# Performance work log

Measured on AMD Instinct MI355X. Metric: run time of the kernel, lower is better.

The kernel has to match this reference:

```python
import jax, jax.numpy as jnp
import numpy as np

K = 20          # neighbors
EPS = 1e-5      # BatchNorm eps (eval mode, running_mean=0, running_var=1)
SLOPE = 0.01    # LeakyReLU default negative_slope


def lrelu(v):
    return jnp.where(v >= 0, v, SLOPE * v)


def bn4d(y, g, b):  # y: (B, C, N, k) or (B, C, N)
    shape = (1, g.shape[0]) + (1,) * (y.ndim - 2)
    return y * (g / jnp.sqrt(1.0 + EPS)).reshape(shape) + b.reshape(shape)


def knn_idx(x, k):  # x: (B, C, N) -> (B, N, k) indices of k nearest points
    xx = jnp.sum(x * x, axis=1)                      # (B, N)
    inner = jnp.einsum('bcn,bcm->bnm', x, x)         # (B, N, N)
    dist = 2.0 * inner - xx[:, :, None] - xx[:, None, :]  # = -||xi-xj||^2
    _, idx = jax.lax.top_k(dist, k)
    return idx


def graph_feature(x, k):  # x: (B, C, N) -> (B, 2C, N, k)
    idx = knn_idx(x, k)                              # (B, N, k)
    xt = jnp.transpose(x, (0, 2, 1))                 # (B, N, C)
    nbr = jax.vmap(lambda p, i: p[i])(xt, idx)       # (B, N, k, C) gather
    ctr = xt[:, :, None, :]                          # (B, N, 1, C)
    feat = jnp.concatenate([nbr - ctr, jnp.broadcast_to(ctr, nbr.shape)], axis=-1)
    return jnp.transpose(feat, (0, 3, 1, 2))         # (B, 2C, N, k)


def edge_conv(x, w, g, b, bias=None):  # 1x1 conv + BN(eval) + LeakyReLU + max over k
    f = graph_feature(x, K)                          # (B, 2C, N, k)
    y = jnp.einsum('oc,bcnk->bonk', w, f)
    if bias is not None:
        y = y + bias.reshape(1, -1, 1, 1)
    return jnp.max(lrelu(bn4d(y, g, b)), axis=-1)    # (B, O, N)


def setup_inputs() -> dict:
    key = jax.random.key(0)
    ks = jax.random.split(key, 24)
    W = lambda k_, o, c: jax.random.normal(k_, (o, c), jnp.float32) / np.sqrt(c)
    g = lambda k_, c: 1.0 + 0.1 * jax.random.normal(k_, (c,), jnp.float32)
    bt = lambda k_, c: 0.1 * jax.random.normal(k_, (c,), jnp.float32)
    return {
        'x': jax.random.normal(ks[0], (8, 1024, 3), jnp.float32),
        'conv1_w': W(ks[1], 64, 6), 'conv1_b': bt(ks[2], 64),
        'bn1_g': g(ks[3], 64), 'bn1_b': bt(ks[4], 64),
        'conv2_w': W(ks[5], 64, 128), 'bn2_g': g(ks[6], 64), 'bn2_b': bt(ks[7], 64),
        'conv3_w': W(ks[8], 128, 128), 'bn3_g': g(ks[9], 128), 'bn3_b': bt(ks[10], 128),
        'conv4_w': W(ks[11], 256, 256), 'bn4_g': g(ks[12], 256), 'bn4_b': bt(ks[13], 256),
        'conv5_w': W(ks[14], 1024, 512),
        'lin1_w': W(ks[15], 512, 1024), 'bn6_g': g(ks[16], 512), 'bn6_b': bt(ks[17], 512),
        'lin2_w': W(ks[18], 256, 512), 'lin2_b': bt(ks[19], 256),
        'bn7_g': g(ks[20], 256), 'bn7_b': bt(ks[21], 256),
        'lin3_w': W(ks[22], 40, 256), 'lin3_b': bt(ks[23], 40),
    }


def reference(x, conv1_w, conv1_b, bn1_g, bn1_b, conv2_w, bn2_g, bn2_b,
              conv3_w, bn3_g, bn3_b, conv4_w, bn4_g, bn4_b, conv5_w,
              lin1_w, bn6_g, bn6_b, lin2_w, lin2_b, bn7_g, bn7_b, lin3_w, lin3_b):
    p = jnp.transpose(x, (0, 2, 1))                  # (B, 3, N)
    x1 = edge_conv(p, conv1_w, bn1_g, bn1_b, bias=conv1_b)   # (B, 64, N)
    x2 = edge_conv(x1, conv2_w, bn2_g, bn2_b)                # (B, 64, N)
    x3 = edge_conv(x2, conv3_w, bn3_g, bn3_b)                # (B, 128, N)
    x4 = edge_conv(x3, conv4_w, bn4_g, bn4_b)                # (B, 256, N)
    xc = jnp.concatenate([x1, x2, x3, x4], axis=1)           # (B, 512, N)
    e = jnp.einsum('oc,bcn->bon', conv5_w, xc)               # (B, 1024, N); bn5 unused in original forward
    gpool = jnp.max(e, axis=-1)                              # (B, 1024) adaptive_max_pool1d(1)
    y = gpool @ lin1_w.T
    y = lrelu(y * (bn6_g / jnp.sqrt(1.0 + EPS)) + bn6_b)     # dropout = identity (eval)
    y = y @ lin2_w.T + lin2_b
    y = lrelu(y * (bn7_g / jnp.sqrt(1.0 + EPS)) + bn7_b)
    return y @ lin3_w.T + lin3_b                             # (B, num_classes)
```

## Files before the change

### kernel.cpp

```cpp
#include <hip/hip_runtime.h>
#include <cmath>
#include <cstdint>
#include <cstddef>

#define NB 8
#define NPTS 1024
#define BN (NB*NPTS)
#define KNN 20
#define XC_C 512
#define BN_SC 0.99999500003749973f

static __device__ __forceinline__ float lrelu(float z) { return z >= 0.f ? z : 0.01f * z; }

template<int CTRL>
static __device__ __forceinline__ void dpp_max2(unsigned& loA, unsigned& hiA,
                                                unsigned& loB, unsigned& hiB) {
    unsigned tlA = (unsigned)__builtin_amdgcn_update_dpp(0, (int)loA, CTRL, 0xF, 0xF, false);
    unsigned thA = (unsigned)__builtin_amdgcn_update_dpp(0, (int)hiA, CTRL, 0xF, 0xF, false);
    unsigned tlB = (unsigned)__builtin_amdgcn_update_dpp(0, (int)loB, CTRL, 0xF, 0xF, false);
    unsigned thB = (unsigned)__builtin_amdgcn_update_dpp(0, (int)hiB, CTRL, 0xF, 0xF, false);
    unsigned long long a = ((unsigned long long)hiA << 32) | loA;
    unsigned long long b = ((unsigned long long)thA << 32) | tlA;
    if (b > a) { loA = tlA; hiA = thA; }
    unsigned long long c = ((unsigned long long)hiB << 32) | loB;
    unsigned long long d = ((unsigned long long)thB << 32) | tlB;
    if (d > c) { loB = tlB; hiB = thB; }
}

static __device__ __forceinline__ void wave_max_u64_x2(unsigned long long vA, unsigned long long vB,
                                                       unsigned long long& winA, unsigned long long& winB) {
    unsigned loA = (unsigned)vA, hiA = (unsigned)(vA >> 32);
    unsigned loB = (unsigned)vB, hiB = (unsigned)(vB >> 32);
    dpp_max2<0x121>(loA, hiA, loB, hiB);
    dpp_max2<0x122>(loA, hiA, loB, hiB);
    dpp_max2<0x124>(loA, hiA, loB, hiB);
    dpp_max2<0x128>(loA, hiA, loB, hiB);
    dpp_max2<0x142>(loA, hiA, loB, hiB);
    dpp_max2<0x143>(loA, hiA, loB, hiB);
    unsigned wloA = (unsigned)__builtin_amdgcn_readlane((int)loA, 63);
    unsigned whiA = (unsigned)__builtin_amdgcn_readlane((int)hiA, 63);
    unsigned wloB = (unsigned)__builtin_amdgcn_readlane((int)loB, 63);
    unsigned whiB = (unsigned)__builtin_amdgcn_readlane((int)hiB, 63);
    winA = ((unsigned long long)whiA << 32) | wloA;
    winB = ((unsigned long long)whiB << 32) | wloB;
}

static __device__ __forceinline__ unsigned long long shflx64(unsigned long long v, int m) {
    int lo = __shfl_xor((int)(unsigned)v, m);
    int hi = __shfl_xor((int)(unsigned)(v >> 32), m);
    return ((unsigned long long)(unsigned)hi << 32) | (unsigned)lo;
}

static __device__ __forceinline__ unsigned long long rdlane64(unsigned long long v, int l) {
    unsigned lo = (unsigned)__builtin_amdgcn_readlane((int)(unsigned)v, l);
    unsigned hi = (unsigned)__builtin_amdgcn_readlane((int)(unsigned)(v >> 32), l);
    return ((unsigned long long)hi << 32) | lo;
}

static __device__ __forceinline__ void bitonic64_desc_x2(unsigned long long& vA,
                                                         unsigned long long& vB, int lane) {
#pragma unroll
    for (int k = 2; k <= 64; k <<= 1) {
#pragma unroll
        for (int j = k >> 1; j > 0; j >>= 1) {
            unsigned long long pA = shflx64(vA, j);
            unsigned long long pB = shflx64(vB, j);
            bool takeMax = (((lane & k) == 0) == ((lane & j) == 0));
            vA = ((pA > vA) == takeMax) ? pA : vA;
            vB = ((pB > vB) == takeMax) ? pB : vB;
        }
    }
}

static __device__ __forceinline__ unsigned short f2bf(float f) {
    unsigned u = __float_as_uint(f);
    unsigned r = u + 0x7fffu + ((u >> 16) & 1u);
    return (unsigned short)(r >> 16);
}
static __device__ __forceinline__ float bf2f(unsigned short h) {
    return __uint_as_float(((unsigned)h) << 16);
}

typedef __attribute__((ext_vector_type(8))) short short8;
typedef __attribute__((ext_vector_type(4))) float floatx4;

__global__ void prep_k(const float* __restrict__ x, float* __restrict__ ft, float* __restrict__ nrm) {
    int i = blockIdx.x * 256 + threadIdx.x;
    if (i >= BN) return;
    int b = i >> 10, n = i & 1023;
    float a = x[3*i], c = x[3*i+1], d = x[3*i+2];
    float* fb = ft + (size_t)b * 3 * NPTS;
    fb[n] = a; fb[NPTS + n] = c; fb[2*NPTS + n] = d;
    nrm[i] = a*a + c*c + d*d;
}

template<int C>
__global__ __launch_bounds__(256) void knn_k(const float* __restrict__ ft,
                                             const float* __restrict__ frow, int frs,
                                             const float* __restrict__ nrm,
                                             int* __restrict__ idx) {
    __shared__ unsigned long long cand[4][2][64];
    int w = threadIdx.x >> 6;
    int lane = threadIdx.x & 63;
    int rA = blockIdx.x * 8 + 2 * w;
    int rB = rA + 1;
    int b = rA >> 10;
    const float* ftb = ft + (size_t)b * C * NPTS;

    float4 accA[4], accB[4];
#pragma unroll
    for (int j = 0; j < 4; j++) { accA[j] = make_float4(0.f,0.f,0.f,0.f); accB[j] = make_float4(0.f,0.f,0.f,0.f); }

    if constexpr ((C & 3) == 0) {
        const float4* crA = (const float4*)(frow + (size_t)rA * frs);
        const float4* crB = (const float4*)(frow + (size_t)rB * frs);
        for (int c4 = 0; c4 < C/4; c4++) {
            float4 ctA = crA[c4], ctB = crB[c4];
#pragma unroll
            for (int cc = 0; cc < 4; cc++) {
                float cA = (&ctA.x)[cc], cB = (&ctB.x)[cc];
                const float4* rm = (const float4*)(ftb + (size_t)(4*c4+cc) * NPTS);
#pragma unroll
                for (int j = 0; j < 4; j++) {
                    float4 v = rm[lane + 64*j];
                    accA[j].x = fmaf(cA, v.x, accA[j].x);
                    accA[j].y = fmaf(cA, v.y, accA[j].y);
                    accA[j].z = fmaf(cA, v.z, accA[j].z);
                    accA[j].w = fmaf(cA, v.w, accA[j].w);
                    accB[j].x = fmaf(cB, v.x, accB[j].x);
                    accB[j].y = fmaf(cB, v.y, accB[j].y);
                    accB[j].z = fmaf(cB, v.z, accB[j].z);
                    accB[j].w = fmaf(cB, v.w, accB[j].w);
                }
            }
        }
    } else {
        for (int c = 0; c < C; c++) {
            float cA = frow[(size_t)rA * frs + c];
            float cB = frow[(size_t)rB * frs + c];
            const float4* rm = (const float4*)(ftb + (size_t)c * NPTS);
#pragma unroll
            for (int j = 0; j < 4; j++) {
                float4 v = rm[lane + 64*j];
                accA[j].x = fmaf(cA, v.x, accA[j].x);
                accA[j].y = fmaf(cA, v.y, accA[j].y);
                accA[j].z = fmaf(cA, v.z, accA[j].z);
                accA[j].w = fmaf(cA, v.w, accA[j].w);
                accB[j].x = fmaf(cB, v.x, accB[j].x);
                accB[j].y = fmaf(cB, v.y, accB[j].y);
                accB[j].z = fmaf(cB, v.z, accB[j].z);
                accB[j].w = fmaf(cB, v.w, accB[j].w);
            }
        }
    }

    unsigned long long keyA[16], keyB[16];
    const float4* nm4 = (const float4*)(nrm + b * NPTS);
#pragma unroll
    for (int j = 0; j < 4; j++) {
        float4 nm = nm4[lane + 64*j];
#pragma unroll
        for (int q = 0; q < 4; q++) {
            int m = 4*(lane + 64*j) + q;
            float fA = 2.f * (&accA[j].x)[q] - (&nm.x)[q];
            unsigned uA = __float_as_uint(fA);
            unsigned sA_ = (unsigned)((int)uA >> 31);
            uA ^= (sA_ | 0x80000000u);
            keyA[4*j+q] = ((unsigned long long)uA << 32) | (unsigned)(1023 - m);
            float fB = 2.f * (&accB[j].x)[q] - (&nm.x)[q];
            unsigned uB = __float_as_uint(fB);
            unsigned sB_ = (unsigned)((int)uB >> 31);
            uB ^= (sB_ | 0x80000000u);
            keyB[4*j+q] = ((unsigned long long)uB << 32) | (unsigned)(1023 - m);
        }
    }

    unsigned long long hA = keyA[0], hB = keyB[0];
#pragma unroll
    for (int i = 1; i < 16; i++) {
        hA = keyA[i] > hA ? keyA[i] : hA;
        hB = keyB[i] > hB ? keyB[i] : hB;
    }

    unsigned long long shA = hA, shB = hB;
    bitonic64_desc_x2(shA, shB, lane);
    unsigned long long LA = rdlane64(shA, KNN - 1);
    unsigned long long LB = rdlane64(shB, KNN - 1);

    int cA = 0, cB = 0;
#pragma unroll
    for (int i = 0; i < 16; i++) {
        cA += (keyA[i] >= LA) ? 1 : 0;
        cB += (keyB[i] >= LB) ? 1 : 0;
    }
    int sA = cA, sB = cB;
#pragma unroll
    for (int off = 1; off < 64; off <<= 1) {
        int tA = __shfl_up(sA, off);
        int tB = __shfl_up(sB, off);
        if (lane >= off) { sA += tA; sB += tB; }
    }
    int totA = __builtin_amdgcn_readlane(sA, 63);
    int totB = __builtin_amdgcn_readlane(sB, 63);
    int pA = sA - cA, pB = sB - cB;

    if (totA <= 64 && totB <= 64) {
        unsigned long long (*cw)[64] = cand[w];
        int wa = pA, wb = pB;
#pragma unroll
        for (int i = 0; i < 16; i++) {
            if (keyA[i] >= LA) cw[0][wa++] = keyA[i];
            if (keyB[i] >= LB) cw[1][wb++] = keyB[i];
        }
        asm volatile("s_waitcnt lgkmcnt(0)" ::: "memory");
        unsigned long long vA = 0ull, vB = 0ull;
        if (lane < totA) vA = cw[0][lane];
        if (lane < totB) vB = cw[1][lane];
        bitonic64_desc_x2(vA, vB, lane);
        if (lane < KNN) {
            idx[rA * KNN + lane] = 1023 - (int)(unsigned)vA;
            idx[rB * KNN + lane] = 1023 - (int)(unsigned)vB;
        }
    } else {
#pragma unroll
        for (int ksz = 2; ksz <= 16; ksz <<= 1) {
#pragma unroll
            for (int jst = ksz >> 1; jst > 0; jst >>= 1) {
#pragma unroll
                for (int i = 0; i < 16; i++) {
                    int l = i ^ jst;
                    if (l > i) {
                        bool dsc = (i & ksz) == 0;
                        unsigned long long a = keyA[i], bbv = keyA[l];
                        bool swA = dsc ? (a < bbv) : (a > bbv);
                        if (swA) { keyA[i] = bbv; keyA[l] = a; }
                        unsigned long long c = keyB[i], d = keyB[l];
                        bool swB = dsc ? (c < d) : (c > d);
                        if (swB) { keyB[i] = d; keyB[l] = c; }
                    }
                }
            }
        }
        int mineA = 0, mineB = 0;
        for (int kk = 0; kk < KNN; kk++) {
            unsigned long long winA, winB;
            wave_max_u64_x2(keyA[0], keyB[0], winA, winB);
            if (lane == kk) {
                mineA = 1023 - (int)(unsigned)winA;
                mineB = 1023 - (int)(unsigned)winB;
            }
            bool popA = (keyA[0] == winA);
            bool popB = (keyB[0] == winB);
#pragma unroll
            for (int t = 0; t < 15; t++) {
                keyA[t] = popA ? keyA[t+1] : keyA[t];
                keyB[t] = popB ? keyB[t+1] : keyB[t];
            }
            keyA[15] = popA ? 0ull : keyA[15];
            keyB[15] = popB ? 0ull : keyB[15];
        }
        if (lane < KNN) {
            idx[rA * KNN + lane] = mineA;
            idx[rB * KNN + lane] = mineB;
        }
    }
}

template<int C, int O, bool HASB, int RPB>
__global__ void hc_k(const float* __restrict__ F, int FS,
                     const float* __restrict__ w, const float* __restrict__ bias,
                     float* __restrict__ Ht, float* __restrict__ Ct) {
    int r0 = blockIdx.x * RPB;
    int o = threadIdx.x;
    const float* wr = w + (size_t)o * (2*C);
    float h[RPB], a2[RPB];
#pragma unroll
    for (int nn = 0; nn < RPB; nn++) { h[nn] = 0.f; a2[nn] = 0.f; }
    if constexpr ((C & 3) == 0) {
        const float4* w1 = (const float4*)wr;
        const float4* w2 = (const float4*)(wr + C);
#pragma unroll 4
        for (int c4 = 0; c4 < C/4; c4++) {
            float4 wa = w1[c4], wb = w2[c4];
#pragma unroll
            for (int nn = 0; nn < RPB; nn++) {
                float4 f = *(const float4*)(F + (size_t)(r0+nn)*FS + 4*c4);
                h[nn]  = fmaf(wa.x,f.x, fmaf(wa.y,f.y, fmaf(wa.z,f.z, fmaf(wa.w,f.w, h[nn]))));
                a2[nn] = fmaf(wb.x,f.x, fmaf(wb.y,f.y, fmaf(wb.z,f.z, fmaf(wb.w,f.w, a2[nn]))));
            }
        }
    } else {
        for (int c = 0; c < C; c++) {
            float wa = wr[c], wb = wr[C+c];
#pragma unroll
            for (int nn = 0; nn < RPB; nn++) {
                float f = F[(size_t)(r0+nn)*FS + c];
                h[nn]  = fmaf(wa, f, h[nn]);
                a2[nn] = fmaf(wb, f, a2[nn]);
            }
        }
    }
    float bs = 0.f;
    if constexpr (HASB) bs = bias[o];
#pragma unroll
    for (int nn = 0; nn < RPB; nn++) {
        size_t ro = (size_t)(r0+nn)*O + o;
        Ht[ro] = h[nn];
        Ct[ro] = a2[nn] - h[nn] + bs;
    }
}

template<int O, bool WFT>
__global__ void gmax_k(const float* __restrict__ Ht, const float* __restrict__ Ct,
                       const int* __restrict__ idx,
                       const float* __restrict__ g, const float* __restrict__ bb,
                       float* __restrict__ xcs, float* __restrict__ ft, float* __restrict__ nrm) {
    int r = blockIdx.x;
    int b = r >> 10, n = r & 1023;
    int o = threadIdx.x;
    const int* id = idx + r * KNN;
    float vmax = -INFINITY, vmin = INFINITY;
    const float* hb = Ht + (size_t)b * NPTS * O + o;
#pragma unroll 4
    for (int k = 0; k < KNN; k++) {
        int m = id[k];
        float v = hb[(size_t)m * O];
        vmax = fmaxf(vmax, v); vmin = fminf(vmin, v);
    }
    float ct = Ct[(size_t)r * O + o];
    float s = g[o] * BN_SC;
    float pre = (s >= 0.f ? vmax : vmin) + ct;
    float out = lrelu(fmaf(s, pre, bb[o]));
    xcs[(size_t)r * XC_C + o] = out;
    if constexpr (WFT) {
        ft[((size_t)b * O + o) * NPTS + n] = out;
        float sq = out * out;
#pragma unroll
        for (int off = 32; off > 0; off >>= 1) sq += __shfl_xor(sq, off);
        __shared__ float red[O/64 > 0 ? O/64 : 1];
        if ((o & 63) == 0) red[o >> 6] = sq;
        __syncthreads();
        if (o == 0) {
            float t = 0.f;
#pragma unroll
            for (int i = 0; i < O/64; i++) t += red[i];
            nrm[r] = t;
        }
    }
}

__global__ void xcvt_k(const float* __restrict__ xc,
                       unsigned short* __restrict__ xh, unsigned short* __restrict__ xl) {
    int i = blockIdx.x * 256 + threadIdx.x;
    float v = xc[i];
    unsigned short h = f2bf(v);
    xh[i] = h;
    xl[i] = f2bf(v - bf2f(h));
}

__global__ void wcvt_k(const float* __restrict__ w5,
                       unsigned short* __restrict__ wh, unsigned short* __restrict__ wl) {
    int i = blockIdx.x * 256 + threadIdx.x;
    float v = w5[i];
    unsigned short h = f2bf(v);
    wh[i] = h;
    wl[i] = f2bf(v - bf2f(h));
}

__global__ __launch_bounds__(256) void conv5mfma_k(const unsigned short* __restrict__ xh,
                                                   const unsigned short* __restrict__ xl,
                                                   const unsigned short* __restrict__ wh,
                                                   const unsigned short* __restrict__ wl,
                                                   float* __restrict__ part) {
    __shared__ short ah_s[32*72];
    __shared__ short al_s[32*72];
    __shared__ short bh_s[128*72];
    __shared__ short bl_s[128*72];
    int b = blockIdx.z, og = blockIdx.y, nt = blockIdx.x;
    int tid = threadIdx.x;
    int w = tid >> 6, lane = tid & 63;
    int m = lane & 15, quad = lane >> 4;
    int h = w >> 1, q = w & 1;
    size_t nbase = (size_t)b * NPTS + nt * 32;
    int obase = og * 128;
    int srow = tid >> 3;
    int scol = (tid & 7) * 8;

    floatx4 acc[4];
#pragma unroll
    for (int t = 0; t < 4; t++) acc[t] = (floatx4){0.f, 0.f, 0.f, 0.f};

    for (int kc = 0; kc < 512; kc += 64) {
        __syncthreads();
        *(short8*)(ah_s + srow*72 + scol) = *(const short8*)(xh + (nbase + srow)*512 + kc + scol);
        *(short8*)(al_s + srow*72 + scol) = *(const short8*)(xl + (nbase + srow)*512 + kc + scol);
#pragma unroll
        for (int i = 0; i < 4; i++) {
            int r = srow + i*32;
            *(short8*)(bh_s + r*72 + scol) = *(const short8*)(wh + (size_t)(obase + r)*512 + kc + scol);
            *(short8*)(bl_s + r*72 + scol) = *(const short8*)(wl + (size_t)(obase + r)*512 + kc + scol);
        }
        __syncthreads();
#pragma unroll
        for (int kk = 0; kk < 2; kk++) {
            short8 ah8 = *(const short8*)(ah_s + (h*16 + m)*72 + kk*32 + quad*8);
            short8 al8 = *(const short8*)(al_s + (h*16 + m)*72 + kk*32 + quad*8);
#pragma unroll
            for (int t = 0; t < 4; t++) {
                short8 bh8 = *(const short8*)(bh_s + (q*64 + t*16 + m)*72 + kk*32 + quad*8);
                short8 bl8 = *(const short8*)(bl_s + (q*64 + t*16 + m)*72 + kk*32 + quad*8);
                acc[t] = __builtin_amdgcn_mfma_f32_16x16x32_bf16(ah8, bh8, acc[t], 0, 0, 0);
                acc[t] = __builtin_amdgcn_mfma_f32_16x16x32_bf16(ah8, bl8, acc[t], 0, 0, 0);
                acc[t] = __builtin_amdgcn_mfma_f32_16x16x32_bf16(al8, bh8, acc[t], 0, 0, 0);
            }
        }
    }
#pragma unroll
    for (int t = 0; t < 4; t++) {
        float v = fmaxf(fmaxf(acc[t][0], acc[t][1]), fmaxf(acc[t][2], acc[t][3]));
        v = fmaxf(v, __shfl_xor(v, 16));
        v = fmaxf(v, __shfl_xor(v, 32));
        if (quad == 0)
            part[((size_t)b * 64 + nt*2 + h) * 1024 + obase + q*64 + t*16 + m] = v;
    }
}

__global__ void gpool_k(const float* __restrict__ part, float* __restrict__ gp) {
    int i = blockIdx.x * 256 + threadIdx.x;
    int b = i >> 10, o = i & 1023;
    const float* pb = part + (size_t)b * 64 * 1024 + o;
    float m = pb[0];
#pragma unroll 4
    for (int j = 1; j < 64; j++) m = fmaxf(m, pb[(size_t)j * 1024]);
    gp[i] = m;
}

template<int C, bool HASBIAS, bool ACT>
__global__ __launch_bounds__(256) void lin_k(const float* __restrict__ X, int xs,
                                             const float* __restrict__ W,
                                             const float* __restrict__ bias,
                                             const float* __restrict__ g, const float* __restrict__ bb,
                                             float* __restrict__ Y, int ys) {
    int wid = (blockIdx.x * 256 + threadIdx.x) >> 6;
    int lane = threadIdx.x & 63;
    int o = wid >> 3;
    int b = wid & 7;
    const float4* wr = (const float4*)(W + (size_t)o * C);
    const float4* xr = (const float4*)(X + (size_t)b * xs);
    float acc = 0.f;
#pragma unroll
    for (int i = 0; i < C/256; i++) {
        float4 w = wr[lane + 64*i];
        float4 xv = xr[lane + 64*i];
        acc = fmaf(w.x,xv.x, fmaf(w.y,xv.y, fmaf(w.z,xv.z, fmaf(w.w,xv.w, acc))));
    }
#pragma unroll
    for (int off = 32; off > 0; off >>= 1) acc += __shfl_xor(acc, off);
    if (lane == 0) {
        if constexpr (HASBIAS) acc += bias[o];
        if constexpr (ACT) acc = lrelu(fmaf(acc, g[o] * BN_SC, bb[o]));
        Y[(size_t)b * ys + o] = acc;
    }
}

extern "C" void kernel_launch(void* const* d_in, const int* in_sizes, int n_in,
                              void* d_out, int out_size, void* d_ws, size_t ws_size,
                              hipStream_t stream) {
    const float* x       = (const float*)d_in[0];
    const float* conv1_w = (const float*)d_in[1];
    const float* conv1_b = (const float*)d_in[2];
    const float* bn1_g   = (const float*)d_in[3];
    const float* bn1_b   = (const float*)d_in[4];
    const float* conv2_w = (const float*)d_in[5];
    const float* bn2_g   = (const float*)d_in[6];
    const float* bn2_b   = (const float*)d_in[7];
    const float* conv3_w = (const float*)d_in[8];
    const float* bn3_g   = (const float*)d_in[9];
    const float* bn3_b   = (const float*)d_in[10];
    const float* conv4_w = (const float*)d_in[11];
    const float* bn4_g   = (const float*)d_in[12];
    const float* bn4_b   = (const float*)d_in[13];
    const float* conv5_w = (const float*)d_in[14];
    const float* lin1_w  = (const float*)d_in[15];
    const float* bn6_g   = (const float*)d_in[16];
    const float* bn6_b   = (const float*)d_in[17];
    const float* lin2_w  = (const float*)d_in[18];
    const float* lin2_b  = (const float*)d_in[19];
    const float* bn7_g   = (const float*)d_in[20];
    const float* bn7_b   = (const float*)d_in[21];
    const float* lin3_w  = (const float*)d_in[22];
    const float* lin3_b  = (const float*)d_in[23];
    float* outp = (float*)d_out;

    float* ws   = (float*)d_ws;
    float* xc   = ws;
    int*   idxb = (int*)(ws + 4194304);
    float* nrm  = ws + 4194304 + 163840;
    float* ft   = nrm + 8192;
    float* part = ft + 1048576;
    float* w5t  = part + 524288;
    float* Ht   = w5t + 524288;
    float* Ct   = Ht + 2097152;
    float* gp   = ft;
    float* y1   = ft + 8192;
    float* y2   = ft + 8192 + 4096;
    unsigned short* xhp = (unsigned short*)Ht;
    unsigned short* xlp = (unsigned short*)Ct;
    unsigned short* whp = (unsigned short*)w5t;
    unsigned short* wlp = whp + 1024*512;

    prep_k<<<BN/256, 256, 0, stream>>>(x, ft, nrm);

    knn_k<3><<<BN/8, 256, 0, stream>>>(ft, x, 3, nrm, idxb);
    hc_k<3, 64, true, 4><<<BN/4, 64, 0, stream>>>(x, 3, conv1_w, conv1_b, Ht, Ct);
    gmax_k<64, true><<<BN, 64, 0, stream>>>(Ht, Ct, idxb, bn1_g, bn1_b, xc + 0, ft, nrm);

    knn_k<64><<<BN/8, 256, 0, stream>>>(ft, xc + 0, XC_C, nrm, idxb);
    hc_k<64, 64, false, 4><<<BN/4, 64, 0, stream>>>(xc + 0, XC_C, conv2_w, nullptr, Ht, Ct);
    gmax_k<64, true><<<BN, 64, 0, stream>>>(Ht, Ct, idxb, bn2_g, bn2_b, xc + 64, ft, nrm);

    knn_k<64><<<BN/8, 256, 0, stream>>>(ft, xc + 64, XC_C, nrm, idxb);
    hc_k<64, 128, false, 4><<<BN/4, 128, 0, stream>>>(xc + 64, XC_C, conv3_w, nullptr, Ht, Ct);
    gmax_k<128, true><<<BN, 128, 0, stream>>>(Ht, Ct, idxb, bn3_g, bn3_b, xc + 128, ft, nrm);

    knn_k<128><<<BN/8, 256, 0, stream>>>(ft, xc + 128, XC_C, nrm, idxb);
    hc_k<128, 256, false, 8><<<BN/8, 256, 0, stream>>>(xc + 128, XC_C, conv4_w, nullptr, Ht, Ct);
    gmax_k<256, false><<<BN, 256, 0, stream>>>(Ht, Ct, idxb, bn4_g, bn4_b, xc + 256, nullptr, nullptr);

    xcvt_k<<<BN*512/256, 256, 0, stream>>>(xc, xhp, xlp);
    wcvt_k<<<1024*512/256, 256, 0, stream>>>(conv5_w, whp, wlp);
    conv5mfma_k<<<dim3(32, 8, NB), 256, 0, stream>>>(xhp, xlp, whp, wlp, part);
    gpool_k<<<NB*1024/256, 256, 0, stream>>>(part, gp);
    lin_k<1024, false, true><<<NB*512/4, 256, 0, stream>>>(gp, 1024, lin1_w, nullptr, bn6_g, bn6_b, y1, 512);
    lin_k<512,  true,  true><<<NB*256/4, 256, 0, stream>>>(y1, 512, lin2_w, lin2_b, bn7_g, bn7_b, y2, 256);
    lin_k<256,  true, false><<<NB*40/4,  256, 0, stream>>>(y2, 256, lin3_w, lin3_b, nullptr, nullptr, outp, 40);
}
```

Baseline: 478.7 us.

## Stage kNN feature chunks in LDS with register prefetch and larger blocks

The kNN distance kernel now uses 512-thread blocks covering 16 query rows. It stages 8-channel chunks of the point features in shared memory, prefetching the next chunk into registers while computing on the current one. Each global feature row is now loaded once per block and shared across 8 waves, where before every wave read it directly from global/L2. The cost is 32KB of LDS per block, two barriers per chunk, and half as many blocks, which could limit occupancy. The C=3 path keeps the old direct loads but runs with the new block shape.

```diff
diff --git a/kernel.cpp b/kernel.cpp
--- a/kernel.cpp
+++ b/kernel.cpp
@@ -95,14 +95,16 @@
 }
 
 template<int C>
-__global__ __launch_bounds__(256) void knn_k(const float* __restrict__ ft,
-                                             const float* __restrict__ frow, int frs,
-                                             const float* __restrict__ nrm,
-                                             int* __restrict__ idx) {
-    __shared__ unsigned long long cand[4][2][64];
-    int w = threadIdx.x >> 6;
-    int lane = threadIdx.x & 63;
-    int rA = blockIdx.x * 8 + 2 * w;
+__global__ __launch_bounds__(512, 4) void knn_k(const float* __restrict__ ft,
+                                                const float* __restrict__ frow, int frs,
+                                                const float* __restrict__ nrm,
+                                                int* __restrict__ idx) {
+    __shared__ float sbuf[8 * NPTS];
+    __shared__ unsigned long long cand[8][2][64];
+    int tid = threadIdx.x;
+    int w = tid >> 6;
+    int lane = tid & 63;
+    int rA = blockIdx.x * 16 + 2 * w;
     int rB = rA + 1;
     int b = rA >> 10;
     const float* ftb = ft + (size_t)b * C * NPTS;
@@ -111,27 +113,49 @@
 #pragma unroll
     for (int j = 0; j < 4; j++) { accA[j] = make_float4(0.f,0.f,0.f,0.f); accB[j] = make_float4(0.f,0.f,0.f,0.f); }
 
-    if constexpr ((C & 3) == 0) {
+    if constexpr ((C % 8) == 0) {
+        constexpr int NCH = C / 8;
         const float4* crA = (const float4*)(frow + (size_t)rA * frs);
         const float4* crB = (const float4*)(frow + (size_t)rB * frs);
-        for (int c4 = 0; c4 < C/4; c4++) {
-            float4 ctA = crA[c4], ctB = crB[c4];
-#pragma unroll
-            for (int cc = 0; cc < 4; cc++) {
-                float cA = (&ctA.x)[cc], cB = (&ctB.x)[cc];
-                const float4* rm = (const float4*)(ftb + (size_t)(4*c4+cc) * NPTS);
-#pragma unroll
-                for (int j = 0; j < 4; j++) {
-                    float4 v = rm[lane + 64*j];
-                    accA[j].x = fmaf(cA, v.x, accA[j].x);
-                    accA[j].y = fmaf(cA, v.y, accA[j].y);
-                    accA[j].z = fmaf(cA, v.z, accA[j].z);
-                    accA[j].w = fmaf(cA, v.w, accA[j].w);
-                    accB[j].x = fmaf(cB, v.x, accB[j].x);
-                    accB[j].y = fmaf(cB, v.y, accB[j].y);
-                    accB[j].z = fmaf(cB, v.z, accB[j].z);
-                    accB[j].w = fmaf(cB, v.w, accB[j].w);
+        const float4* src4 = (const float4*)ftb;
+        float4* sb4 = (float4*)sbuf;
+        float4 pf[4];
+#pragma unroll
+        for (int i = 0; i < 4; i++) pf[i] = src4[i*512 + tid];
+#pragma unroll
+        for (int i = 0; i < 4; i++) sb4[i*512 + tid] = pf[i];
+        __syncthreads();
+        for (int ch = 0; ch < NCH; ch++) {
+            if (ch + 1 < NCH) {
+#pragma unroll
+                for (int i = 0; i < 4; i++) pf[i] = src4[(size_t)(ch+1)*2048 + i*512 + tid];
+            }
+#pragma unroll
+            for (int cc4 = 0; cc4 < 2; cc4++) {
+                float4 ctA = crA[ch*2 + cc4], ctB = crB[ch*2 + cc4];
+#pragma unroll
+                for (int cc = 0; cc < 4; cc++) {
+                    float cA = (&ctA.x)[cc], cB = (&ctB.x)[cc];
+                    const float4* rm = (const float4*)(sbuf + (size_t)(cc4*4 + cc) * NPTS);
+#pragma unroll
+                    for (int j = 0; j < 4; j++) {
+                        float4 v = rm[lane + 64*j];
+                        accA[j].x = fmaf(cA, v.x, accA[j].x);
+                        accA[j].y = fmaf(cA, v.y, accA[j].y);
+                        accA[j].z = fmaf(cA, v.z, accA[j].z);
+                        accA[j].w = fmaf(cA, v.w, accA[j].w);
+                        accB[j].x = fmaf(cB, v.x, accB[j].x);
+                        accB[j].y = fmaf(cB, v.y, accB[j].y);
+                        accB[j].z = fmaf(cB, v.z, accB[j].z);
+                        accB[j].w = fmaf(cB, v.w, accB[j].w);
+                    }
                 }
+            }
+            if (ch + 1 < NCH) {
+                __syncthreads();
+#pragma unroll
+                for (int i = 0; i < 4; i++) sb4[i*512 + tid] = pf[i];
+                __syncthreads();
             }
         }
     } else {
@@ -511,19 +535,19 @@
 
     prep_k<<<BN/256, 256, 0, stream>>>(x, ft, nrm);
 
-    knn_k<3><<<BN/8, 256, 0, stream>>>(ft, x, 3, nrm, idxb);
+    knn_k<3><<<BN/16, 512, 0, stream>>>(ft, x, 3, nrm, idxb);
     hc_k<3, 64, true, 4><<<BN/4, 64, 0, stream>>>(x, 3, conv1_w, conv1_b, Ht, Ct);
     gmax_k<64, true><<<BN, 64, 0, stream>>>(Ht, Ct, idxb, bn1_g, bn1_b, xc + 0, ft, nrm);
 
-    knn_k<64><<<BN/8, 256, 0, stream>>>(ft, xc + 0, XC_C, nrm, idxb);
+    knn_k<64><<<BN/16, 512, 0, stream>>>(ft, xc + 0, XC_C, nrm, idxb);
     hc_k<64, 64, false, 4><<<BN/4, 64, 0, stream>>>(xc + 0, XC_C, conv2_w, nullptr, Ht, Ct);
     gmax_k<64, true><<<BN, 64, 0, stream>>>(Ht, Ct, idxb, bn2_g, bn2_b, xc + 64, ft, nrm);
 
-    knn_k<64><<<BN/8, 256, 0, stream>>>(ft, xc + 64, XC_C, nrm, idxb);
+    knn_k<64><<<BN/16, 512, 0, stream>>>(ft, xc + 64, XC_C, nrm, idxb);
     hc_k<64, 128, false, 4><<<BN/4, 128, 0, stream>>>(xc + 64, XC_C, conv3_w, nullptr, Ht, Ct);
     gmax_k<128, true><<<BN, 128, 0, stream>>>(Ht, Ct, idxb, bn3_g, bn3_b, xc + 128, ft, nrm);
 
-    knn_k<128><<<BN/8, 256, 0, stream>>>(ft, xc + 128, XC_C, nrm, idxb);
+    knn_k<128><<<BN/16, 512, 0, stream>>>(ft, xc + 128, XC_C, nrm, idxb);
     hc_k<128, 256, false, 8><<<BN/8, 256, 0, stream>>>(xc + 128, XC_C, conv4_w, nullptr, Ht, Ct);
     gmax_k<256, false><<<BN, 256, 0, stream>>>(Ht, Ct, idxb, bn4_g, bn4_b, xc + 256, nullptr, nullptr);
 
```

Result: slower. 641.6 us (+34.0%).
